# Optimization experiments

Measured on AMD Instinct MI355X. Metric: run time of the kernel, lower is better.

The kernel has to match this reference:

```python
import jax, jax.numpy as jnp
import numpy as np

D_MODEL = 1024
NUM_HEADS = 16
HEAD_DIM = D_MODEL // NUM_HEADS


def setup_inputs() -> dict:
    key = jax.random.key(0)
    ks = jax.random.split(key, 11)
    B, S = 2, 2048
    scale = 1.0 / np.sqrt(D_MODEL)
    inp = {
        "q": jax.random.normal(ks[0], (B, S, D_MODEL), jnp.float32),
        "k": jax.random.normal(ks[1], (B, S, D_MODEL), jnp.float32),
        "v": jax.random.normal(ks[2], (B, S, D_MODEL), jnp.float32),
        "Wq": jax.random.normal(ks[3], (D_MODEL, D_MODEL), jnp.float32) * scale,
        "bq": jnp.zeros((D_MODEL,), jnp.float32),
        "Wk": jax.random.normal(ks[4], (D_MODEL, D_MODEL), jnp.float32) * scale,
        "bk": jnp.zeros((D_MODEL,), jnp.float32),
        "Wv": jax.random.normal(ks[5], (D_MODEL, D_MODEL), jnp.float32) * scale,
        "bv": jnp.zeros((D_MODEL,), jnp.float32),
        "Wo": jax.random.normal(ks[6], (D_MODEL, D_MODEL), jnp.float32) * scale,
        "bo": jnp.zeros((D_MODEL,), jnp.float32),
    }
    return inp


def reference(q, k, v, Wq, bq, Wk, bk, Wv, bv, Wo, bo):
    B, S, _ = q.shape
    # Linear projections (torch Linear: x @ W.T + b), split into heads -> [b,h,s,d]
    def proj(x, W, b):
        y = jnp.einsum('bsm,nm->bsn', x, W) + b
        return y.reshape(B, -1, NUM_HEADS, HEAD_DIM).transpose(0, 2, 1, 3)
    qh = proj(q, Wq, bq)
    kh = proj(k, Wk, bk)
    vh = proj(v, Wv, bv)
    # NOTE: source scales by sqrt(d_model), NOT sqrt(head_dim) -- faithful quirk
    factor = jnp.sqrt(jnp.float32(D_MODEL))
    scores = jnp.einsum('bhqd,bhkd->bhqk', qh, kh) / factor
    attn = jax.nn.softmax(scores, axis=-1)
    out = jnp.einsum('bhqk,bhkd->bhqd', attn, vh)
    out = out.transpose(0, 2, 1, 3).reshape(B, S, D_MODEL)
    # out projection; dropout=0.0 (eval) is identity
    return jnp.einsum('bsm,nm->bsn', out, Wo) + bo
```

## Files before the change

kernel.cpp:

```cpp
#include <hip/hip_runtime.h>
#include <hip/hip_bf16.h>

typedef __hip_bfloat16 bf16;
typedef short short8 __attribute__((ext_vector_type(8)));
typedef short bs4 __attribute__((ext_vector_type(4)));
typedef float f32x4 __attribute__((ext_vector_type(4)));

#define MFMA_BF16(a, b, c) __builtin_amdgcn_mfma_f32_16x16x32_bf16(a, b, c, 0, 0, 0)
#define MFMA16_BF16(a, b, c) __builtin_amdgcn_mfma_f32_16x16x16bf16_1k(a, b, c, 0, 0, 0)

#define QSCALE 0.045084439f

__device__ __forceinline__ void async_copy16(const bf16* g, bf16* l) {
    __builtin_amdgcn_global_load_lds(
        (const __attribute__((address_space(1))) unsigned int*)(const void*)g,
        (__attribute__((address_space(3))) unsigned int*)(void*)l, 16, 0, 0);
}

__global__ __launch_bounds__(256) void convert_all(
    const float* __restrict__ q, const float* __restrict__ k, const float* __restrict__ v,
    const float* __restrict__ wq, const float* __restrict__ wk,
    const float* __restrict__ wv, const float* __restrict__ wo,
    bf16* __restrict__ qb, bf16* __restrict__ kb, bf16* __restrict__ vb,
    bf16* __restrict__ wqb, bf16* __restrict__ wkb, bf16* __restrict__ wvb,
    bf16* __restrict__ wob)
{
    int blk = blockIdx.x;
    const float* s; bf16* d; int rel;
    if      (blk < 1024) { s = q;  d = qb;  rel = blk; }
    else if (blk < 2048) { s = k;  d = kb;  rel = blk - 1024; }
    else if (blk < 3072) { s = v;  d = vb;  rel = blk - 2048; }
    else if (blk < 3328) { s = wq; d = wqb; rel = blk - 3072; }
    else if (blk < 3584) { s = wk; d = wkb; rel = blk - 3328; }
    else if (blk < 3840) { s = wv; d = wvb; rel = blk - 3584; }
    else                 { s = wo; d = wob; rel = blk - 3840; }
    size_t base = (size_t)rel * 1024 + threadIdx.x;
#pragma unroll
    for (int i = 0; i < 4; i++) {
        float4 f = ((const float4*)s)[base + i * 256];
        union { bf16 h[4]; uint2 u; } pk;
        pk.h[0] = (bf16)f.x; pk.h[1] = (bf16)f.y;
        pk.h[2] = (bf16)f.z; pk.h[3] = (bf16)f.w;
        ((uint2*)d)[base + i * 256] = pk.u;
    }
}

__global__ __launch_bounds__(256) void gemm_qkv(
    const bf16* __restrict__ qb, const bf16* __restrict__ kb, const bf16* __restrict__ vb,
    const bf16* __restrict__ wqb, const bf16* __restrict__ wkb, const bf16* __restrict__ wvb,
    const float* __restrict__ bq, const float* __restrict__ bk, const float* __restrict__ bv,
    bf16* __restrict__ Qp, bf16* __restrict__ Kp, bf16* __restrict__ Vt)
{
    __shared__ bf16 Al[128 * 64];
    __shared__ bf16 Bl[128 * 64];

    const int sel = blockIdx.y >> 3;
    const bf16* A; const bf16* W; const float* bias;
    if      (sel == 0) { A = qb; W = wqb; bias = bq; }
    else if (sel == 1) { A = kb; W = wkb; bias = bk; }
    else               { A = vb; W = wvb; bias = bv; }

    const int K = 1024, N = 1024;
    const int t = threadIdx.x;
    const int lane = t & 63, wave = t >> 6;
    const int ln = lane & 15, quad = lane >> 4;
    const int wm = wave >> 1, wn = wave & 1;
    const int m0 = blockIdx.x * 128, n0 = (blockIdx.y & 7) * 128;

    f32x4 acc[4][4];
#pragma unroll
    for (int i = 0; i < 4; i++)
#pragma unroll
        for (int j = 0; j < 4; j++) acc[i][j] = (f32x4){0.f, 0.f, 0.f, 0.f};

    const int lk = ln & 7;
    const int srow = t >> 3, sidx0 = t & 7;

    for (int k0 = 0; k0 < K; k0 += 64) {
        const bf16* Ab = A + (size_t)m0 * K + k0;
        const bf16* Wb = W + (size_t)n0 * K + k0;
#pragma unroll
        for (int p = 0; p < 4; p++) {
            int row = p * 32 + srow, idx = sidx0 ^ (row & 7);
            async_copy16(Ab + (size_t)row * K + idx * 8, &Al[(p * 256 + wave * 64) * 8]);
        }
#pragma unroll
        for (int p = 0; p < 4; p++) {
            int row = p * 32 + srow, idx = sidx0 ^ (row & 7);
            async_copy16(Wb + (size_t)row * K + idx * 8, &Bl[(p * 256 + wave * 64) * 8]);
        }
        __syncthreads();

#pragma unroll
        for (int kk = 0; kk < 2; kk++) {
            short8 af[4], bfr[4];
#pragma unroll
            for (int i = 0; i < 4; i++) {
                int r = wm * 64 + i * 16 + ln;
                af[i] = *(const short8*)&Al[r * 64 + (((kk << 2) | quad) ^ lk) * 8];
            }
#pragma unroll
            for (int j = 0; j < 4; j++) {
                int r = wn * 64 + j * 16 + ln;
                bfr[j] = *(const short8*)&Bl[r * 64 + (((kk << 2) | quad) ^ lk) * 8];
            }
#pragma unroll
            for (int i = 0; i < 4; i++)
#pragma unroll
                for (int j = 0; j < 4; j++)
                    acc[i][j] = MFMA_BF16(af[i], bfr[j], acc[i][j]);
        }
        __syncthreads();
    }

#pragma unroll
    for (int j = 0; j < 4; j++) {
        int c = n0 + wn * 64 + j * 16 + ln;
        float bv2 = bias[c];
        if (sel == 2) {
            int h = c >> 6, dd = c & 63;
#pragma unroll
            for (int i = 0; i < 4; i++) {
                int m = m0 + wm * 64 + i * 16 + quad * 4;
                int bb = m >> 11, s = m & 2047;
                union { bf16 h4[4]; uint2 u; } pk;
#pragma unroll
                for (int r = 0; r < 4; r++) pk.h4[r] = (bf16)(acc[i][j][r] + bv2);
                *(uint2*)&Vt[(((size_t)(bb * 16 + h)) * 64 + dd) * 2048 + s] = pk.u;
            }
        } else {
            bf16* out = (sel == 0) ? Qp : Kp;
            float scl = (sel == 0) ? QSCALE : 1.0f;
#pragma unroll
            for (int i = 0; i < 4; i++) {
                int rb = m0 + wm * 64 + i * 16 + quad * 4;
#pragma unroll
                for (int r = 0; r < 4; r++)
                    out[(size_t)(rb + r) * N + c] = (bf16)((acc[i][j][r] + bv2) * scl);
            }
        }
    }
}

__global__ __launch_bounds__(256) void gemm_fin(
    const bf16* __restrict__ A, const bf16* __restrict__ W,
    const float* __restrict__ bias, float* __restrict__ C)
{
    __shared__ bf16 Al[128 * 64];
    __shared__ bf16 Bl[64 * 64];

    const int K = 1024, N = 1024;
    const int t = threadIdx.x;
    const int lane = t & 63, wave = t >> 6;
    const int ln = lane & 15, quad = lane >> 4;
    const int wm = wave >> 1, wn = wave & 1;
    const int m0 = blockIdx.x * 128, n0 = blockIdx.y * 64;

    f32x4 acc[4][2];
#pragma unroll
    for (int i = 0; i < 4; i++)
#pragma unroll
        for (int j = 0; j < 2; j++) acc[i][j] = (f32x4){0.f, 0.f, 0.f, 0.f};

    const int lk = ln & 7;
    const int srow = t >> 3, sidx0 = t & 7;

    for (int k0 = 0; k0 < K; k0 += 64) {
        const bf16* Ab = A + (size_t)m0 * K + k0;
        const bf16* Wb = W + (size_t)n0 * K + k0;
#pragma unroll
        for (int p = 0; p < 4; p++) {
            int row = p * 32 + srow, idx = sidx0 ^ (row & 7);
            async_copy16(Ab + (size_t)row * K + idx * 8, &Al[(p * 256 + wave * 64) * 8]);
        }
#pragma unroll
        for (int p = 0; p < 2; p++) {
            int row = p * 32 + srow, idx = sidx0 ^ (row & 7);
            async_copy16(Wb + (size_t)row * K + idx * 8, &Bl[(p * 256 + wave * 64) * 8]);
        }
        __syncthreads();

#pragma unroll
        for (int kk = 0; kk < 2; kk++) {
            short8 af[4], bfr[2];
#pragma unroll
            for (int i = 0; i < 4; i++) {
                int r = wm * 64 + i * 16 + ln;
                af[i] = *(const short8*)&Al[r * 64 + (((kk << 2) | quad) ^ lk) * 8];
            }
#pragma unroll
            for (int j = 0; j < 2; j++) {
                int r = wn * 32 + j * 16 + ln;
                bfr[j] = *(const short8*)&Bl[r * 64 + (((kk << 2) | quad) ^ lk) * 8];
            }
#pragma unroll
            for (int i = 0; i < 4; i++)
#pragma unroll
                for (int j = 0; j < 2; j++)
                    acc[i][j] = MFMA_BF16(af[i], bfr[j], acc[i][j]);
        }
        __syncthreads();
    }

#pragma unroll
    for (int j = 0; j < 2; j++) {
        int c = n0 + wn * 32 + j * 16 + ln;
        float bv2 = bias[c];
#pragma unroll
        for (int i = 0; i < 4; i++) {
            int rb = m0 + wm * 64 + i * 16 + quad * 4;
#pragma unroll
            for (int r = 0; r < 4; r++)
                C[(size_t)(rb + r) * N + c] = acc[i][j][r] + bv2;
        }
    }
}

__global__ __launch_bounds__(256) void attn128q(
    const bf16* __restrict__ Q, const bf16* __restrict__ K,
    const bf16* __restrict__ V, bf16* __restrict__ O)
{
    const int S = 2048, D = 1024;
    __shared__ bf16 Kl[2][128 * 64];
    __shared__ bf16 Vl[2][64 * 128];

    const int t = threadIdx.x, lane = t & 63, wave = t >> 6;
    const int ln = lane & 15, quad = lane >> 4;
    const int h = blockIdx.x & 15, b = blockIdx.x >> 4, qt = blockIdx.y;
    const size_t kqbase = (size_t)b * S * D + (size_t)h * 64;
    const size_t vbase = ((size_t)(b * 16 + h)) * 64 * 2048;

    short8 aq[2][2];
#pragma unroll
    for (int g = 0; g < 2; g++) {
        const bf16* qp = Q + kqbase + (size_t)(qt * 128 + g * 64 + wave * 16 + ln) * D;
        aq[g][0] = *(const short8*)(qp + quad * 8);
        aq[g][1] = *(const short8*)(qp + 32 + quad * 8);
    }
    asm volatile("" :: "v"(aq[0][0]), "v"(aq[0][1]), "v"(aq[1][0]), "v"(aq[1][1]));

    f32x4 o[2][4];
    float l[2] = {0.f, 0.f};
#pragma unroll
    for (int g = 0; g < 2; g++)
#pragma unroll
        for (int i = 0; i < 4; i++) o[g][i] = (f32x4){0.f, 0.f, 0.f, 0.f};

    const int lk = ln & 7;
    const int kof0 = ln * 64 + ((quad ^ lk) * 8);
    const int kof1 = ln * 64 + (((4 | quad) ^ lk) * 8);
    int vof[8];
#pragma unroll
    for (int nk = 0; nk < 8; nk++)
        vof[nk] = ln * 128 + (((nk * 2 + (quad >> 1)) ^ lk) * 8 + (quad & 1) * 4);

    const int krow = t >> 3, kidx = t & 7;
    const int vrow = t >> 4, vidx = t & 15;

#define STAGE_KV(buf_, kt_) do {                                               \
    _Pragma("unroll")                                                          \
    for (int p = 0; p < 4; p++) {                                              \
        int row = p * 32 + krow, idx = kidx ^ (row & 7);                       \
        async_copy16(K + kqbase + (size_t)((kt_) * 128 + row) * D + idx * 8,   \
                     &Kl[buf_][(p * 256 + wave * 64) * 8]);                    \
    }                                                                          \
    _Pragma("unroll")                                                          \
    for (int p = 0; p < 4; p++) {                                              \
        int row = p * 16 + vrow, idx = vidx ^ (row & 7);                       \
        async_copy16(V + vbase + (size_t)row * 2048 + (kt_) * 128 + idx * 8,   \
                     &Vl[buf_][(p * 256 + wave * 64) * 8]);                    \
    }                                                                          \
} while (0)

    STAGE_KV(0, 0);

    for (int kt = 0; kt < S / 128; kt++) {
        const int cur = kt & 1;
        if (kt < S / 128 - 1) {
            STAGE_KV(cur ^ 1, kt + 1);
            asm volatile("s_waitcnt vmcnt(8)" ::: "memory");
        } else {
            asm volatile("s_waitcnt vmcnt(0)" ::: "memory");
        }
        __builtin_amdgcn_s_barrier();

        const bf16* Klc = Kl[cur];
        const bf16* Vlc = Vl[cur];

#pragma unroll
        for (int nk = 0; nk < 8; nk++) {
            short8 kf0 = *(const short8*)&Klc[nk * 1024 + kof0];
            short8 kf1 = *(const short8*)&Klc[nk * 1024 + kof1];

            __builtin_amdgcn_s_setprio(1);
            f32x4 a0 = (f32x4){0.f, 0.f, 0.f, 0.f};
            f32x4 a1 = (f32x4){0.f, 0.f, 0.f, 0.f};
            a0 = MFMA_BF16(kf0, aq[0][0], a0);
            a1 = MFMA_BF16(kf0, aq[1][0], a1);
            a0 = MFMA_BF16(kf1, aq[0][1], a0);
            a1 = MFMA_BF16(kf1, aq[1][1], a1);
            __builtin_amdgcn_s_setprio(0);

            bs4 pa[2];
            {
                union { bs4 s4; bf16 hh[4]; } pk0, pk1;
#pragma unroll
                for (int r = 0; r < 4; r++) {
                    float p0 = __builtin_amdgcn_exp2f(a0[r]);
                    float p1 = __builtin_amdgcn_exp2f(a1[r]);
                    l[0] += p0; l[1] += p1;
                    pk0.hh[r] = (bf16)p0; pk1.hh[r] = (bf16)p1;
                }
                pa[0] = pk0.s4; pa[1] = pk1.s4;
            }

            __builtin_amdgcn_s_setprio(1);
#pragma unroll
            for (int nd = 0; nd < 4; nd++) {
                bs4 vb = *(const bs4*)&Vlc[nd * 2048 + vof[nk]];
                o[0][nd] = MFMA16_BF16(pa[0], vb, o[0][nd]);
                o[1][nd] = MFMA16_BF16(pa[1], vb, o[1][nd]);
            }
            __builtin_amdgcn_s_setprio(0);
        }

        asm volatile("" ::: "memory");
        __builtin_amdgcn_s_barrier();
    }
#undef STAGE_KV

#pragma unroll
    for (int g = 0; g < 2; g++) {
        float lv = l[g];
        lv += __shfl_xor(lv, 16);
        lv += __shfl_xor(lv, 32);
#pragma unroll
        for (int r = 0; r < 4; r++) {
            float inv = __builtin_amdgcn_rcpf(__shfl(lv, quad * 4 + r));
            int row = qt * 128 + g * 64 + wave * 16 + quad * 4 + r;
#pragma unroll
            for (int nd = 0; nd < 4; nd++)
                O[((size_t)b * S + row) * D + h * 64 + nd * 16 + ln] =
                    (bf16)(o[g][nd][r] * inv);
        }
    }
}

extern "C" void kernel_launch(void* const* d_in, const int* in_sizes, int n_in,
                              void* d_out, int out_size, void* d_ws, size_t ws_size,
                              hipStream_t stream) {
    (void)in_sizes; (void)n_in; (void)out_size; (void)ws_size;
    const float* q  = (const float*)d_in[0];
    const float* k  = (const float*)d_in[1];
    const float* v  = (const float*)d_in[2];
    const float* Wq = (const float*)d_in[3];
    const float* bq = (const float*)d_in[4];
    const float* Wk = (const float*)d_in[5];
    const float* bk = (const float*)d_in[6];
    const float* Wv = (const float*)d_in[7];
    const float* bv = (const float*)d_in[8];
    const float* Wo = (const float*)d_in[9];
    const float* bo = (const float*)d_in[10];
    float* out = (float*)d_out;

    const int M = 4096, N = 1024;
    const size_t MN = (size_t)M * N;
    const size_t NN = (size_t)N * N;
    bf16* qb  = (bf16*)d_ws;
    bf16* kb  = qb + MN;
    bf16* vb  = kb + MN;
    bf16* wqb = vb + MN;
    bf16* wkb = wqb + NN;
    bf16* wvb = wkb + NN;
    bf16* wob = wvb + NN;
    bf16* Qp  = wob + NN;
    bf16* Kp  = Qp + MN;
    bf16* Vt  = Kp + MN;
    bf16* AO  = qb;

    dim3 blk(256);
    convert_all<<<4096, blk, 0, stream>>>(q, k, v, Wq, Wk, Wv, Wo,
                                          qb, kb, vb, wqb, wkb, wvb, wob);

    gemm_qkv<<<dim3(32, 24), blk, 0, stream>>>(qb, kb, vb, wqb, wkb, wvb,
                                               bq, bk, bv, Qp, Kp, Vt);

    attn128q<<<dim3(32, 16), blk, 0, stream>>>(Qp, Kp, Vt, AO);

    gemm_fin<<<dim3(32, 16), blk, 0, stream>>>(AO, wob, bo, out);
}
```

Before: 225.4 us.

## Double attention block to 512 threads with one 16-row query group per wave

The attention kernel now launches 8 waves per block instead of 4. Each wave owns a single 16-row query slice instead of two, and the K/V staging loads are split across the extra waves, with the async-copy wait count adjusted to match. The goal is more resident waves and lower register pressure, so LDS and MFMA latency are hidden better. In exchange, each K/V fragment read from LDS feeds only one query group per wave, which doubles LDS read traffic per unit of compute.

```diff
diff --git a/kernel.cpp b/kernel.cpp
--- a/kernel.cpp
+++ b/kernel.cpp
@@ -216,7 +216,7 @@
     }
 }
 
-__global__ __launch_bounds__(256) void attn128q(
+__global__ __launch_bounds__(512) void attn128q(
     const bf16* __restrict__ Q, const bf16* __restrict__ K,
     const bf16* __restrict__ V, bf16* __restrict__ O)
 {
@@ -230,21 +230,18 @@
     const size_t kqbase = (size_t)b * S * D + (size_t)h * 64;
     const size_t vbase = ((size_t)(b * 16 + h)) * 64 * 2048;
 
-    short8 aq[2][2];
-#pragma unroll
-    for (int g = 0; g < 2; g++) {
-        const bf16* qp = Q + kqbase + (size_t)(qt * 128 + g * 64 + wave * 16 + ln) * D;
-        aq[g][0] = *(const short8*)(qp + quad * 8);
-        aq[g][1] = *(const short8*)(qp + 32 + quad * 8);
-    }
-    asm volatile("" :: "v"(aq[0][0]), "v"(aq[0][1]), "v"(aq[1][0]), "v"(aq[1][1]));
-
-    f32x4 o[2][4];
-    float l[2] = {0.f, 0.f};
-#pragma unroll
-    for (int g = 0; g < 2; g++)
-#pragma unroll
-        for (int i = 0; i < 4; i++) o[g][i] = (f32x4){0.f, 0.f, 0.f, 0.f};
+    short8 aq0, aq1;
+    {
+        const bf16* qp = Q + kqbase + (size_t)(qt * 128 + wave * 16 + ln) * D;
+        aq0 = *(const short8*)(qp + quad * 8);
+        aq1 = *(const short8*)(qp + 32 + quad * 8);
+    }
+    asm volatile("" :: "v"(aq0), "v"(aq1));
+
+    f32x4 o[4];
+    f32x4 l4 = (f32x4){0.f, 0.f, 0.f, 0.f};
+#pragma unroll
+    for (int i = 0; i < 4; i++) o[i] = (f32x4){0.f, 0.f, 0.f, 0.f};
 
     const int lk = ln & 7;
     const int kof0 = ln * 64 + ((quad ^ lk) * 8);
@@ -259,16 +256,16 @@
 
 #define STAGE_KV(buf_, kt_) do {                                               \
     _Pragma("unroll")                                                          \
-    for (int p = 0; p < 4; p++) {                                              \
-        int row = p * 32 + krow, idx = kidx ^ (row & 7);                       \
+    for (int p = 0; p < 2; p++) {                                              \
+        int row = p * 64 + krow, idx = kidx ^ (row & 7);                       \
         async_copy16(K + kqbase + (size_t)((kt_) * 128 + row) * D + idx * 8,   \
-                     &Kl[buf_][(p * 256 + wave * 64) * 8]);                    \
+                     &Kl[buf_][(p * 512 + wave * 64) * 8]);                    \
     }                                                                          \
     _Pragma("unroll")                                                          \
-    for (int p = 0; p < 4; p++) {                                              \
-        int row = p * 16 + vrow, idx = vidx ^ (row & 7);                       \
+    for (int p = 0; p < 2; p++) {                                              \
+        int row = p * 32 + vrow, idx = vidx ^ (row & 7);                       \
         async_copy16(V + vbase + (size_t)row * 2048 + (kt_) * 128 + idx * 8,   \
-                     &Vl[buf_][(p * 256 + wave * 64) * 8]);                    \
+                     &Vl[buf_][(p * 512 + wave * 64) * 8]);                    \
     }                                                                          \
 } while (0)
 
@@ -278,7 +275,7 @@
         const int cur = kt & 1;
         if (kt < S / 128 - 1) {
             STAGE_KV(cur ^ 1, kt + 1);
-            asm volatile("s_waitcnt vmcnt(8)" ::: "memory");
+            asm volatile("s_waitcnt vmcnt(4)" ::: "memory");
         } else {
             asm volatile("s_waitcnt vmcnt(0)" ::: "memory");
         }
@@ -293,33 +290,29 @@
             short8 kf1 = *(const short8*)&Klc[nk * 1024 + kof1];
 
             __builtin_amdgcn_s_setprio(1);
-            f32x4 a0 = (f32x4){0.f, 0.f, 0.f, 0.f};
-            f32x4 a1 = (f32x4){0.f, 0.f, 0.f, 0.f};
-            a0 = MFMA_BF16(kf0, aq[0][0], a0);
-            a1 = MFMA_BF16(kf0, aq[1][0], a1);
-            a0 = MFMA_BF16(kf1, aq[0][1], a0);
-            a1 = MFMA_BF16(kf1, aq[1][1], a1);
+            f32x4 a = (f32x4){0.f, 0.f, 0.f, 0.f};
+            a = MFMA_BF16(kf0, aq0, a);
+            a = MFMA_BF16(kf1, aq1, a);
             __builtin_amdgcn_s_setprio(0);
 
-            bs4 pa[2];
+            bs4 pa;
             {
-                union { bs4 s4; bf16 hh[4]; } pk0, pk1;
+                union { bs4 s4; bf16 hh[4]; } pk;
+                f32x4 p;
 #pragma unroll
                 for (int r = 0; r < 4; r++) {
-                    float p0 = __builtin_amdgcn_exp2f(a0[r]);
-                    float p1 = __builtin_amdgcn_exp2f(a1[r]);
-                    l[0] += p0; l[1] += p1;
-                    pk0.hh[r] = (bf16)p0; pk1.hh[r] = (bf16)p1;
+                    p[r] = __builtin_amdgcn_exp2f(a[r]);
+                    pk.hh[r] = (bf16)p[r];
                 }
-                pa[0] = pk0.s4; pa[1] = pk1.s4;
+                l4 += p;
+                pa = pk.s4;
             }
 
             __builtin_amdgcn_s_setprio(1);
 #pragma unroll
             for (int nd = 0; nd < 4; nd++) {
                 bs4 vb = *(const bs4*)&Vlc[nd * 2048 + vof[nk]];
-                o[0][nd] = MFMA16_BF16(pa[0], vb, o[0][nd]);
-                o[1][nd] = MFMA16_BF16(pa[1], vb, o[1][nd]);
+                o[nd] = MFMA16_BF16(pa, vb, o[nd]);
             }
             __builtin_amdgcn_s_setprio(0);
         }
@@ -329,19 +322,18 @@
     }
 #undef STAGE_KV
 
-#pragma unroll
-    for (int g = 0; g < 2; g++) {
-        float lv = l[g];
+    {
+        float lv = (l4[0] + l4[1]) + (l4[2] + l4[3]);
         lv += __shfl_xor(lv, 16);
         lv += __shfl_xor(lv, 32);
 #pragma unroll
         for (int r = 0; r < 4; r++) {
             float inv = __builtin_amdgcn_rcpf(__shfl(lv, quad * 4 + r));
-            int row = qt * 128 + g * 64 + wave * 16 + quad * 4 + r;
+            int row = qt * 128 + wave * 16 + quad * 4 + r;
 #pragma unroll
             for (int nd = 0; nd < 4; nd++)
                 O[((size_t)b * S + row) * D + h * 64 + nd * 16 + ln] =
-                    (bf16)(o[g][nd][r] * inv);
+                    (bf16)(o[nd][r] * inv);
         }
     }
 }
@@ -385,7 +377,7 @@
     gemm_qkv<<<dim3(32, 24), blk, 0, stream>>>(qb, kb, vb, wqb, wkb, wvb,
                                                bq, bk, bv, Qp, Kp, Vt);
 
-    attn128q<<<dim3(32, 16), blk, 0, stream>>>(Qp, Kp, Vt, AO);
+    attn128q<<<dim3(32, 16), dim3(512), 0, stream>>>(Qp, Kp, Vt, AO);
 
     gemm_fin<<<dim3(32, 16), blk, 0, stream>>>(AO, wob, bo, out);
 }
```

Measured after the change: 221.4 us. No clear change (-1.8%).
